# Performance work log

Hardware: AMD Instinct MI355X
Metric: run time of the kernel (lower is better)

## Reference

```python
import jax, jax.numpy as jnp
import numpy as np

S, C, H, D = 4096, 2048, 16, 128  # seq, channels, heads, head_dim
EPS = 1.1920929e-07  # torch F.rms_norm default eps = finfo(float32).eps


def setup_inputs() -> dict:
    key = jax.random.key(0)
    ks = jax.random.split(key, 12)
    w = 0.02
    return {
        "x": jax.random.normal(ks[0], (S, C), dtype=jnp.float32),
        "rope": jax.random.normal(ks[1], (S, 1, D // 2, 2, 2), dtype=jnp.float32),
        "Wq": jax.random.normal(ks[2], (C, C), dtype=jnp.float32) * w,
        "bq": jnp.zeros((C,), dtype=jnp.float32),
        "Wk": jax.random.normal(ks[3], (C, C), dtype=jnp.float32) * w,
        "bk": jnp.zeros((C,), dtype=jnp.float32),
        "Wv": jax.random.normal(ks[4], (C, C), dtype=jnp.float32) * w,
        "bv": jnp.zeros((C,), dtype=jnp.float32),
        "qn_w": jnp.ones((D,), dtype=jnp.float32),
        "kn_w": jnp.ones((D,), dtype=jnp.float32),
        "Wo": jax.random.normal(ks[5], (C, C), dtype=jnp.float32) * w,
        "bo": jnp.zeros((C,), dtype=jnp.float32),
    }


def _rms_norm(x, weight):
    # RMSNorm over last dim, as F.rms_norm
    inv = jax.lax.rsqrt(jnp.mean(x * x, axis=-1, keepdims=True) + EPS)
    return x * inv * weight


def _apply_rotary(x, rope):
    # x: [S, H, D]; rope: [S, 1, D//2, 2, 2]
    s, h, d = x.shape
    x_ = x.reshape(s, h, d // 2, 1, 2)
    out = (rope * x_).sum(axis=-1)  # [S, H, D//2, 2]
    return out.reshape(s, h, d)


def reference(x, rope, Wq, bq, Wk, bk, Wv, bv, qn_w, kn_w, Wo, bo):
    # QKV projections -> [S, H, D]
    q = (x @ Wq.T + bq).reshape(S, H, D)
    k = (x @ Wk.T + bk).reshape(S, H, D)
    v = (x @ Wv.T + bv).reshape(S, H, D)
    # RMSNorm on q/k per head_dim
    q = _rms_norm(q, qn_w)
    k = _rms_norm(k, kn_w)
    # Custom rotary (table-driven 2x2 rotation)
    q = _apply_rotary(q, rope)
    k = _apply_rotary(k, rope)
    # Dense scaled dot-product attention over seq, per head
    scale = 1.0 / jnp.sqrt(jnp.asarray(D, dtype=q.dtype))
    scores = jnp.einsum("shd,thd->hst", q, k) * scale  # [H, S, S]
    probs = jax.nn.softmax(scores, axis=-1)
    out = jnp.einsum("hst,thd->shd", probs, v).reshape(S, C)
    return out @ Wo.T + bo
```

## Files before the change

### kernel.cpp

```cpp
#include <hip/hip_runtime.h>

#define S 4096
#define C 2048
#define H 16
#define D 128
#define EPS 1.1920929e-07f
#define QSCALE (0.08838834764831845f * 1.4426950408889634f)

typedef __attribute__((ext_vector_type(8))) short short8;
typedef __attribute__((ext_vector_type(4))) float f32x4;
typedef __attribute__((ext_vector_type(4))) unsigned int uint4v;

#if __has_builtin(__builtin_amdgcn_exp2f)
#define EXP2F __builtin_amdgcn_exp2f
#else
#define EXP2F exp2f
#endif

__device__ __forceinline__ unsigned short f2bf(float f) {
  unsigned int u = __builtin_bit_cast(unsigned int, f);
  u += 0x7fff + ((u >> 16) & 1);
  return (unsigned short)(u >> 16);
}
__device__ __forceinline__ float bf2f(unsigned short v) {
  unsigned int u = ((unsigned int)v) << 16;
  return __builtin_bit_cast(float, u);
}
__device__ __forceinline__ unsigned int pkbf(float a, float b) {
  return (unsigned int)f2bf(a) | ((unsigned int)f2bf(b) << 16);
}
__device__ __forceinline__ unsigned int pkbf_trunc(float a, float b) {
  return __builtin_amdgcn_perm(__builtin_bit_cast(unsigned int, b),
                               __builtin_bit_cast(unsigned int, a), 0x07060302);
}
__device__ __forceinline__ float lo16f(unsigned int d) {
  return __builtin_bit_cast(float, d << 16);
}
__device__ __forceinline__ float hi16f(unsigned int d) {
  return __builtin_bit_cast(float, d & 0xffff0000u);
}
__device__ __forceinline__ void gld16(const unsigned short* g, unsigned short* l) {
  __builtin_amdgcn_global_load_lds(
      (const __attribute__((address_space(1))) unsigned int*)g,
      (__attribute__((address_space(3))) unsigned int*)l, 16, 0, 0);
}
__device__ __forceinline__ short8 mk_a(unsigned int a, unsigned int b,
                                       unsigned int c, unsigned int d) {
  uint4v u;
  u[0] = a; u[1] = b; u[2] = c; u[3] = d;
  return __builtin_bit_cast(short8, u);
}

__global__ void cvt_kernel(const float* __restrict__ src,
                           unsigned short* __restrict__ dst, int n) {
  int i = (blockIdx.x * 256 + threadIdx.x) * 4;
  if (i >= n) return;
  float4 v = *(const float4*)(src + i);
  ushort4 o;
  o.x = f2bf(v.x); o.y = f2bf(v.y); o.z = f2bf(v.z); o.w = f2bf(v.w);
  *(ushort4*)(dst + i) = o;
}
__global__ void cvtw_kernel(const float* __restrict__ w0, const float* __restrict__ w1,
                            const float* __restrict__ w2, const float* __restrict__ w3,
                            unsigned short* __restrict__ dst) {
  const float* srcs[4] = {w0, w1, w2, w3};
  const float* src = srcs[blockIdx.y];
  int i = (blockIdx.x * 256 + threadIdx.x) * 4;
  float4 v = *(const float4*)(src + i);
  ushort4 o;
  o.x = f2bf(v.x); o.y = f2bf(v.y); o.z = f2bf(v.z); o.w = f2bf(v.w);
  *(ushort4*)(dst + (size_t)blockIdx.y * C * C + i) = o;
}
__global__ void bias_concat(const float* __restrict__ bq, const float* __restrict__ bk,
                            const float* __restrict__ bv, float* __restrict__ dst) {
  int i = blockIdx.x * 256 + threadIdx.x;
  const float* s = (i < C) ? bq : ((i < 2 * C) ? bk : bv);
  dst[i] = s[i & (C - 1)];
}

__global__ __launch_bounds__(256) void gemm_bt(const unsigned short* __restrict__ A,
                                               const unsigned short* __restrict__ B,
                                               const float* __restrict__ bias,
                                               float* __restrict__ outf,
                                               unsigned short* __restrict__ qh,
                                               unsigned short* __restrict__ kh,
                                               unsigned short* __restrict__ vt,
                                               int N, int mode) {
  __shared__ __align__(16) unsigned short U[128 * 136];
  unsigned short* Al = U;
  unsigned short* Bl = U + 128 * 64;
  const int t = threadIdx.x, w = t >> 6, lane = t & 63;
  const int lq = lane & 15, quad = lane >> 4;
  const int wm = w & 1, wn = w >> 1;
  const int m0 = blockIdx.y * 128, n0 = blockIdx.x * 128;
  f32x4 acc[4][4] = {};
  float biasv[4];
#pragma unroll
  for (int nt = 0; nt < 4; nt++) biasv[nt] = bias[n0 + wn * 64 + nt * 16 + lq];
  const int sr = lane >> 3, sg = lane & 7;
  for (int k0 = 0; k0 < C; k0 += 64) {
    __syncthreads();
#pragma unroll
    for (int p = 0; p < 4; p++) {
      int row = w * 32 + p * 8 + sr;
      int c = sg ^ (row & 7);
      gld16(A + (size_t)(m0 + row) * C + k0 + c * 8, &Al[(w * 32 + p * 8) * 64]);
      gld16(B + (size_t)(n0 + row) * C + k0 + c * 8, &Bl[(w * 32 + p * 8) * 64]);
    }
    __syncthreads();
#pragma unroll
    for (int ks = 0; ks < 2; ks++) {
      short8 af[4], bf[4];
#pragma unroll
      for (int mt = 0; mt < 4; mt++) {
        int row = wm * 64 + mt * 16 + lq;
        af[mt] = *(const short8*)&Al[row * 64 + ((ks * 4 + quad) ^ (lq & 7)) * 8];
      }
#pragma unroll
      for (int nt = 0; nt < 4; nt++) {
        int row = wn * 64 + nt * 16 + lq;
        bf[nt] = *(const short8*)&Bl[row * 64 + ((ks * 4 + quad) ^ (lq & 7)) * 8];
      }
#pragma unroll
      for (int mt = 0; mt < 4; mt++)
#pragma unroll
        for (int nt = 0; nt < 4; nt++)
          acc[mt][nt] = __builtin_amdgcn_mfma_f32_16x16x32_bf16(af[mt], bf[nt], acc[mt][nt], 0, 0, 0);
    }
  }

  if (mode == 0) {
#pragma unroll
    for (int mt = 0; mt < 4; mt++)
#pragma unroll
      for (int nt = 0; nt < 4; nt++) {
        int n = n0 + wn * 64 + nt * 16 + lq;
#pragma unroll
        for (int r = 0; r < 4; r++) {
          int m = m0 + wm * 64 + mt * 16 + quad * 4 + r;
          outf[(size_t)m * N + n] = acc[mt][nt][r] + biasv[nt];
        }
      }
    return;
  }

  const int gh = n0 >> 7;
  __syncthreads();
  const int rr = t >> 4, ck = t & 15;
  if (gh < 32) {
#pragma unroll
    for (int mt = 0; mt < 4; mt++)
#pragma unroll
      for (int nt = 0; nt < 4; nt++) {
        int dloc = wn * 64 + nt * 16 + lq;
#pragma unroll
        for (int r = 0; r < 4; r++)
          U[(wm * 64 + mt * 16 + quad * 4 + r) * 136 + dloc] = f2bf(acc[mt][nt][r] + biasv[nt]);
      }
    __syncthreads();
    unsigned short* dst = ((gh < 16) ? qh : kh) + (size_t)(gh & 15) * S * D;
#pragma unroll
    for (int p = 0; p < 8; p++) {
      int m = p * 16 + rr;
      uint4 vv = *(const uint4*)&U[m * 136 + ck * 8];
      *(uint4*)(dst + (size_t)(m0 + m) * D + ck * 8) = vv;
    }
  } else {
    #pragma unroll
    for (int mt = 0; mt < 4; mt++)
#pragma unroll
      for (int nt = 0; nt < 4; nt++) {
        int dloc = wn * 64 + nt * 16 + lq;
        int mlocP = wm * 64 + (mt >> 1) * 32 + quad * 8 + (mt & 1) * 4;
        *(unsigned int*)&U[dloc * 136 + mlocP] =
            pkbf(acc[mt][nt][0] + biasv[nt], acc[mt][nt][1] + biasv[nt]);
        *(unsigned int*)&U[dloc * 136 + mlocP + 2] =
            pkbf(acc[mt][nt][2] + biasv[nt], acc[mt][nt][3] + biasv[nt]);
      }
    __syncthreads();
    unsigned short* dst = vt + (size_t)(gh - 32) * D * S;
#pragma unroll
    for (int p = 0; p < 8; p++) {
      int d = p * 16 + rr;
      uint4 vv = *(const uint4*)&U[d * 136 + ck * 8];
      *(uint4*)(dst + (size_t)d * S + m0 + ck * 8) = vv;
    }
  }
}

__global__ __launch_bounds__(256) void rmsrope_kernel(unsigned short* __restrict__ qh,
                                                      unsigned short* __restrict__ kh,
                                                      const float* __restrict__ qn_w,
                                                      const float* __restrict__ kn_w,
                                                      const float* __restrict__ rope) {
  const int which = blockIdx.y;
  unsigned short* io = which ? kh : qh;
  const float* wgt = which ? kn_w : qn_w;
  const float scale = which ? 1.0f : QSCALE;
  int wid = (blockIdx.x * 256 + threadIdx.x) >> 6;
  int lane = threadIdx.x & 63;
  int s = wid & (S - 1);
  unsigned short* row = io + (size_t)wid * D;
  unsigned int pr = *(unsigned int*)(row + lane * 2);
  float a = bf2f((unsigned short)(pr & 0xffff));
  float b = bf2f((unsigned short)(pr >> 16));
  float ss = a * a + b * b;
  for (int m = 1; m < 64; m <<= 1) ss += __shfl_xor(ss, m);
  float inv = rsqrtf(ss * (1.0f / 128.0f) + EPS) * scale;
  float2 wv = *(const float2*)(wgt + lane * 2);
  float an = a * inv * wv.x, bn = b * inv * wv.y;
  float4 r = *(const float4*)(rope + (size_t)s * 256 + lane * 4);
  *(unsigned int*)(row + lane * 2) = pkbf(r.x * an + r.y * bn, r.z * an + r.w * bn);
}

__global__ __launch_bounds__(256, 2) void flash_kernel(const unsigned short* __restrict__ qh,
                                                       const unsigned short* __restrict__ kh,
                                                       const unsigned short* __restrict__ vt,
                                                       unsigned short* __restrict__ ao) {
  __shared__ __align__(16) unsigned short Klds[128 * 128];
  __shared__ __align__(16) unsigned short Vlds[128 * 128];
  const int h = blockIdx.y, i0 = blockIdx.x * 128;
  const int t = threadIdx.x, w = t >> 6, lane = t & 63;
  const int lq = lane & 15, quad = lane >> 4;

  const unsigned short* Qbase = qh + ((size_t)h * S + i0 + w * 32 + lq) * D;
  short8 qfrag[2][4];
#pragma unroll
  for (int qi = 0; qi < 2; qi++)
#pragma unroll
    for (int kt = 0; kt < 4; kt++)
      qfrag[qi][kt] = *(const short8*)(Qbase + (size_t)qi * 16 * D + kt * 32 + quad * 8);

  f32x4 oacc[2][8] = {};
  float lrun[2] = {0.0f, 0.0f};
  const unsigned short* Kbase = kh + (size_t)h * S * D;
  const unsigned short* Vbase = vt + (size_t)h * D * S;

  const int kr = lane >> 4, kg = lane & 15;

  for (int j0 = 0; j0 < S; j0 += 128) {
    __syncthreads();
#pragma unroll
    for (int p = 0; p < 8; p++) {
      int krow = w * 32 + p * 4 + kr;
      gld16(Kbase + (size_t)(j0 + krow) * D + (kg ^ (krow & 7)) * 8,
            &Klds[(w * 32 + p * 4) * 128]);
      gld16(Vbase + (size_t)krow * S + j0 + (kg ^ (krow & 7)) * 8,
            &Vlds[(w * 32 + p * 4) * 128]);
    }
    __syncthreads();

    f32x4 sacc[2][8] = {};
    __builtin_amdgcn_s_setprio(1);
#pragma unroll
    for (int kt = 0; kt < 4; kt++)
#pragma unroll
      for (int nt = 0; nt < 8; nt++) {
        int row = nt * 16 + lq;
        short8 af = *(const short8*)&Klds[row * 128 + (((kt * 4 + quad) ^ (row & 7)) * 8)];
        sacc[0][nt] = __builtin_amdgcn_mfma_f32_16x16x32_bf16(af, qfrag[0][kt], sacc[0][nt], 0, 0, 0);
        sacc[1][nt] = __builtin_amdgcn_mfma_f32_16x16x32_bf16(af, qfrag[1][kt], sacc[1][nt], 0, 0, 0);
      }
    __builtin_amdgcn_s_setprio(0);

    unsigned int pd[2][8][2];
#pragma unroll
    for (int qi = 0; qi < 2; qi++) {
      float rsum = 0.0f;
#pragma unroll
      for (int nt = 0; nt < 8; nt++) {
        float e0 = EXP2F(sacc[qi][nt][0]);
        float e1 = EXP2F(sacc[qi][nt][1]);
        float e2 = EXP2F(sacc[qi][nt][2]);
        float e3 = EXP2F(sacc[qi][nt][3]);
        unsigned int d0 = pkbf_trunc(e0, e1);
        unsigned int d1 = pkbf_trunc(e2, e3);
        pd[qi][nt][0] = d0;
        pd[qi][nt][1] = d1;
        rsum += (lo16f(d0) + hi16f(d0)) + (lo16f(d1) + hi16f(d1));
      }
      lrun[qi] += rsum;
    }

    __builtin_amdgcn_s_setprio(1);
#pragma unroll
    for (int kk = 0; kk < 4; kk++) {
      short8 a0 = mk_a(pd[0][2 * kk][0], pd[0][2 * kk][1], pd[0][2 * kk + 1][0], pd[0][2 * kk + 1][1]);
      short8 a1 = mk_a(pd[1][2 * kk][0], pd[1][2 * kk][1], pd[1][2 * kk + 1][0], pd[1][2 * kk + 1][1]);
#pragma unroll
      for (int dt = 0; dt < 8; dt++) {
        int row = dt * 16 + lq;
        short8 bf = *(const short8*)&Vlds[row * 128 + (((kk * 4 + quad) ^ (row & 7)) * 8)];
        oacc[0][dt] = __builtin_amdgcn_mfma_f32_16x16x32_bf16(a0, bf, oacc[0][dt], 0, 0, 0);
        oacc[1][dt] = __builtin_amdgcn_mfma_f32_16x16x32_bf16(a1, bf, oacc[1][dt], 0, 0, 0);
      }
    }
    __builtin_amdgcn_s_setprio(0);
  }

#pragma unroll
  for (int qi = 0; qi < 2; qi++) {
    lrun[qi] += __shfl_xor(lrun[qi], 16);
    lrun[qi] += __shfl_xor(lrun[qi], 32);
  }
  float il[2][4];
#pragma unroll
  for (int qi = 0; qi < 2; qi++)
#pragma unroll
    for (int r = 0; r < 4; r++) il[qi][r] = 1.0f / __shfl(lrun[qi], quad * 4 + r);
#pragma unroll
  for (int qi = 0; qi < 2; qi++)
#pragma unroll
    for (int dt = 0; dt < 8; dt++)
#pragma unroll
      for (int r = 0; r < 4; r++)
        ao[(size_t)(i0 + w * 32 + qi * 16 + quad * 4 + r) * C + h * 128 + dt * 16 + lq] =
            f2bf(oacc[qi][dt][r] * il[qi][r]);
}

extern "C" void kernel_launch(void* const* d_in, const int* in_sizes, int n_in,
                              void* d_out, int out_size, void* d_ws, size_t ws_size,
                              hipStream_t stream) {
  const float* x    = (const float*)d_in[0];
  const float* rope = (const float*)d_in[1];
  const float* Wq   = (const float*)d_in[2];
  const float* bq   = (const float*)d_in[3];
  const float* Wk   = (const float*)d_in[4];
  const float* bk   = (const float*)d_in[5];
  const float* Wv   = (const float*)d_in[6];
  const float* bv   = (const float*)d_in[7];
  const float* qn_w = (const float*)d_in[8];
  const float* kn_w = (const float*)d_in[9];
  const float* Wo   = (const float*)d_in[10];
  const float* bo   = (const float*)d_in[11];
  float* out = (float*)d_out;

  unsigned short* xb  = (unsigned short*)d_ws;
  unsigned short* wqb = xb + (size_t)S * C;
  unsigned short* wob = wqb + (size_t)3 * C * C;
  unsigned short* qh  = wqb + (size_t)4 * C * C;
  unsigned short* kh  = qh + (size_t)S * C;
  unsigned short* vt  = kh + (size_t)S * C;
  unsigned short* ao  = vt + (size_t)S * C;
  float* bqkv = (float*)(ao + (size_t)S * C);

  cvt_kernel<<<S * C / 1024, 256, 0, stream>>>(x, xb, S * C);
  cvtw_kernel<<<dim3(C * C / 1024, 4), 256, 0, stream>>>(Wq, Wk, Wv, Wo, wqb);
  bias_concat<<<3 * C / 256, 256, 0, stream>>>(bq, bk, bv, bqkv);

  gemm_bt<<<dim3(3 * C / 128, S / 128), 256, 0, stream>>>(
      xb, wqb, bqkv, nullptr, qh, kh, vt, 3 * C, 1);

  rmsrope_kernel<<<dim3((H * S) / 4, 2), 256, 0, stream>>>(qh, kh, qn_w, kn_w, rope);

  flash_kernel<<<dim3(S / 128, H), 256, 0, stream>>>(qh, kh, vt, ao);

  gemm_bt<<<dim3(C / 128, S / 128), 256, 0, stream>>>(
      ao, wob, bo, out, nullptr, nullptr, nullptr, C, 0);
}
```

Before: 472.0 us.

## Double-buffer K/V tiles with BN=64 and compute softmax row sums via MFMA

Halves the key tile to 64 rows and double-buffers the K and V tiles in LDS, so the global-to-LDS load of the next tile overlaps the MFMA work on the current one. That removes one of the two barriers per iteration. The scalar row-sum of exponentials and its final cross-lane shuffle reduction are replaced by an extra MFMA against a vector of bf16 ones, which moves the reduction onto the matrix units. The cost is twice as many loop iterations and changed LDS layouts for V.

```diff
diff --git a/kernel.cpp b/kernel.cpp
--- a/kernel.cpp
+++ b/kernel.cpp
@@ -6,6 +6,8 @@
 #define D 128
 #define EPS 1.1920929e-07f
 #define QSCALE (0.08838834764831845f * 1.4426950408889634f)
+#define BN 64
+#define NT (S / BN)
 
 typedef __attribute__((ext_vector_type(8))) short short8;
 typedef __attribute__((ext_vector_type(4))) float f32x4;
@@ -32,12 +34,6 @@
 __device__ __forceinline__ unsigned int pkbf_trunc(float a, float b) {
   return __builtin_amdgcn_perm(__builtin_bit_cast(unsigned int, b),
                                __builtin_bit_cast(unsigned int, a), 0x07060302);
-}
-__device__ __forceinline__ float lo16f(unsigned int d) {
-  return __builtin_bit_cast(float, d << 16);
-}
-__device__ __forceinline__ float hi16f(unsigned int d) {
-  return __builtin_bit_cast(float, d & 0xffff0000u);
 }
 __device__ __forceinline__ void gld16(const unsigned short* g, unsigned short* l) {
   __builtin_amdgcn_global_load_lds(
@@ -217,8 +213,8 @@
                                                        const unsigned short* __restrict__ kh,
                                                        const unsigned short* __restrict__ vt,
                                                        unsigned short* __restrict__ ao) {
-  __shared__ __align__(16) unsigned short Klds[128 * 128];
-  __shared__ __align__(16) unsigned short Vlds[128 * 128];
+  __shared__ __align__(16) unsigned short Klds[2 * BN * D];
+  __shared__ __align__(16) unsigned short Vlds[2 * D * BN];
   const int h = blockIdx.y, i0 = blockIdx.x * 128;
   const int t = threadIdx.x, w = t >> 6, lane = t & 63;
   const int lq = lane & 15, quad = lane >> 4;
@@ -232,65 +228,86 @@
       qfrag[qi][kt] = *(const short8*)(Qbase + (size_t)qi * 16 * D + kt * 32 + quad * 8);
 
   f32x4 oacc[2][8] = {};
-  float lrun[2] = {0.0f, 0.0f};
+  f32x4 dacc[2] = {};
   const unsigned short* Kbase = kh + (size_t)h * S * D;
   const unsigned short* Vbase = vt + (size_t)h * D * S;
 
-  const int kr = lane >> 4, kg = lane & 15;
-
-  for (int j0 = 0; j0 < S; j0 += 128) {
-    __syncthreads();
-#pragma unroll
-    for (int p = 0; p < 8; p++) {
-      int krow = w * 32 + p * 4 + kr;
-      gld16(Kbase + (size_t)(j0 + krow) * D + (kg ^ (krow & 7)) * 8,
-            &Klds[(w * 32 + p * 4) * 128]);
-      gld16(Vbase + (size_t)krow * S + j0 + (kg ^ (krow & 7)) * 8,
-            &Vlds[(w * 32 + p * 4) * 128]);
-    }
-    __syncthreads();
-
-    f32x4 sacc[2][8] = {};
+  const int k_r = lane >> 4, k_g = lane & 15;
+  const int v_r = lane >> 3, v_g = lane & 7;
+
+  uint4v onesu;
+  onesu[0] = 0x3F803F80u; onesu[1] = 0x3F803F80u; onesu[2] = 0x3F803F80u; onesu[3] = 0x3F803F80u;
+  const short8 ones = __builtin_bit_cast(short8, onesu);
+
+#pragma unroll
+  for (int p = 0; p < 4; p++) {
+    int kr = w * 16 + p * 4 + k_r;
+    gld16(Kbase + (size_t)kr * D + (k_g ^ (kr & 7)) * 8, &Klds[(w * 16 + p * 4) * D]);
+  }
+#pragma unroll
+  for (int p = 0; p < 4; p++) {
+    int vr = w * 32 + p * 8 + v_r;
+    gld16(Vbase + (size_t)vr * S + (v_g ^ (vr & 7)) * 8, &Vlds[(w * 32 + p * 8) * BN]);
+  }
+
+  for (int tt = 0; tt < NT; ++tt) {
+    const int cur = tt & 1;
+    unsigned short* Kc = Klds + cur * (BN * D);
+    unsigned short* Vc = Vlds + cur * (D * BN);
+    __syncthreads();
+    if (tt + 1 < NT) {
+      const int j1 = (tt + 1) * BN;
+      unsigned short* Kn = Klds + (cur ^ 1) * (BN * D);
+      unsigned short* Vn = Vlds + (cur ^ 1) * (D * BN);
+#pragma unroll
+      for (int p = 0; p < 4; p++) {
+        int kr = w * 16 + p * 4 + k_r;
+        gld16(Kbase + (size_t)(j1 + kr) * D + (k_g ^ (kr & 7)) * 8, &Kn[(w * 16 + p * 4) * D]);
+      }
+#pragma unroll
+      for (int p = 0; p < 4; p++) {
+        int vr = w * 32 + p * 8 + v_r;
+        gld16(Vbase + (size_t)vr * S + j1 + (v_g ^ (vr & 7)) * 8, &Vn[(w * 32 + p * 8) * BN]);
+      }
+    }
+
+    f32x4 sacc[2][4] = {};
     __builtin_amdgcn_s_setprio(1);
 #pragma unroll
     for (int kt = 0; kt < 4; kt++)
 #pragma unroll
-      for (int nt = 0; nt < 8; nt++) {
+      for (int nt = 0; nt < 4; nt++) {
         int row = nt * 16 + lq;
-        short8 af = *(const short8*)&Klds[row * 128 + (((kt * 4 + quad) ^ (row & 7)) * 8)];
+        short8 af = *(const short8*)&Kc[row * D + (((kt * 4 + quad) ^ (row & 7)) * 8)];
         sacc[0][nt] = __builtin_amdgcn_mfma_f32_16x16x32_bf16(af, qfrag[0][kt], sacc[0][nt], 0, 0, 0);
         sacc[1][nt] = __builtin_amdgcn_mfma_f32_16x16x32_bf16(af, qfrag[1][kt], sacc[1][nt], 0, 0, 0);
       }
     __builtin_amdgcn_s_setprio(0);
 
-    unsigned int pd[2][8][2];
-#pragma unroll
-    for (int qi = 0; qi < 2; qi++) {
-      float rsum = 0.0f;
-#pragma unroll
-      for (int nt = 0; nt < 8; nt++) {
+    unsigned int pd[2][4][2];
+#pragma unroll
+    for (int qi = 0; qi < 2; qi++)
+#pragma unroll
+      for (int nt = 0; nt < 4; nt++) {
         float e0 = EXP2F(sacc[qi][nt][0]);
         float e1 = EXP2F(sacc[qi][nt][1]);
         float e2 = EXP2F(sacc[qi][nt][2]);
         float e3 = EXP2F(sacc[qi][nt][3]);
-        unsigned int d0 = pkbf_trunc(e0, e1);
-        unsigned int d1 = pkbf_trunc(e2, e3);
-        pd[qi][nt][0] = d0;
-        pd[qi][nt][1] = d1;
-        rsum += (lo16f(d0) + hi16f(d0)) + (lo16f(d1) + hi16f(d1));
-      }
-      lrun[qi] += rsum;
-    }
+        pd[qi][nt][0] = pkbf_trunc(e0, e1);
+        pd[qi][nt][1] = pkbf_trunc(e2, e3);
+      }
 
     __builtin_amdgcn_s_setprio(1);
 #pragma unroll
-    for (int kk = 0; kk < 4; kk++) {
+    for (int kk = 0; kk < 2; kk++) {
       short8 a0 = mk_a(pd[0][2 * kk][0], pd[0][2 * kk][1], pd[0][2 * kk + 1][0], pd[0][2 * kk + 1][1]);
       short8 a1 = mk_a(pd[1][2 * kk][0], pd[1][2 * kk][1], pd[1][2 * kk + 1][0], pd[1][2 * kk + 1][1]);
+      dacc[0] = __builtin_amdgcn_mfma_f32_16x16x32_bf16(a0, ones, dacc[0], 0, 0, 0);
+      dacc[1] = __builtin_amdgcn_mfma_f32_16x16x32_bf16(a1, ones, dacc[1], 0, 0, 0);
 #pragma unroll
       for (int dt = 0; dt < 8; dt++) {
         int row = dt * 16 + lq;
-        short8 bf = *(const short8*)&Vlds[row * 128 + (((kk * 4 + quad) ^ (row & 7)) * 8)];
+        short8 bf = *(const short8*)&Vc[row * BN + (((kk * 4 + quad) ^ (row & 7)) * 8)];
         oacc[0][dt] = __builtin_amdgcn_mfma_f32_16x16x32_bf16(a0, bf, oacc[0][dt], 0, 0, 0);
         oacc[1][dt] = __builtin_amdgcn_mfma_f32_16x16x32_bf16(a1, bf, oacc[1][dt], 0, 0, 0);
       }
@@ -298,16 +315,11 @@
     __builtin_amdgcn_s_setprio(0);
   }
 
-#pragma unroll
-  for (int qi = 0; qi < 2; qi++) {
-    lrun[qi] += __shfl_xor(lrun[qi], 16);
-    lrun[qi] += __shfl_xor(lrun[qi], 32);
-  }
   float il[2][4];
 #pragma unroll
   for (int qi = 0; qi < 2; qi++)
 #pragma unroll
-    for (int r = 0; r < 4; r++) il[qi][r] = 1.0f / __shfl(lrun[qi], quad * 4 + r);
+    for (int r = 0; r < 4; r++) il[qi][r] = 1.0f / dacc[qi][r];
 #pragma unroll
   for (int qi = 0; qi < 2; qi++)
 #pragma unroll
```

Result: no change. 463.6 us (-1.8%).
